# Kernel tuning notes

Hardware: AMD Instinct MI355X
Metric: run time of the kernel (lower is better)

## Reference

```python
import jax, jax.numpy as jnp
import numpy as np

B = 16      # number of point clouds in the batch
N = 2048    # points per cloud
P = B * N   # total points (flat PyG-style batching)
K = 16      # neighbors per point (col 0 = self loop)
OUT = 512   # out_channels


def _linear(key, fi, fo):
    # torch nn.Linear default init: U(-1/sqrt(fi), 1/sqrt(fi))
    s = 1.0 / np.sqrt(fi)
    kw, kb = jax.random.split(key)
    W = jax.random.uniform(kw, (fi, fo), jnp.float32, -s, s)
    b = jax.random.uniform(kb, (fo,), jnp.float32, -s, s)
    return W, b


def setup_inputs() -> dict:
    key = jax.random.key(0)
    ks = jax.random.split(key, 6)
    pos = jax.random.normal(ks[0], (P, 3), jnp.float32)
    # flat batch vector: points are grouped contiguously per cloud
    batch = (jnp.arange(P, dtype=jnp.int32) // N).astype(jnp.int32)
    # within-cloud random neighbor indices (stand-in for knn/radius graph)
    base = (jnp.arange(P) // N) * N  # offset of each point's cloud
    nbr = base[:, None] + jax.random.randint(ks[1], (P, K), 0, N)
    nbr = nbr.at[:, 0].set(jnp.arange(P))  # self loop (PyG add_self_loops)
    W1, b1 = _linear(ks[2], 3, 64)          # sa1 MLP layer 1
    W2, b2 = _linear(ks[3], 64, 128)        # sa1 MLP layer 2
    W3, b3 = _linear(ks[4], 128 + 3, 256)   # sa2 MLP layer 1
    W4, b4 = _linear(ks[5], 256, OUT)       # sa2 MLP layer 2
    return dict(pos=pos, nbr=nbr.astype(jnp.int64), batch=batch,
                W1=W1, b1=b1, W2=W2, b2=b2, W3=W3, b3=b3, W4=W4, b4=b4)


def reference(pos, nbr, batch, W1, b1, W2, b2, W3, b3, W4, b4):
    # ----- sa1: x is None -> message = MLP(pos_j - pos_i), max-aggregated -----
    diff = pos[nbr] - pos[:, None, :]                      # [P, K, 3]
    h1 = jnp.maximum(diff @ W1 + b1, 0.0) @ W2 + b2        # [P, K, 128]
    x1 = jnp.max(h1, axis=1)                               # [P, 128]
    # ----- sa2: message = MLP([x1_j, pos_j - pos_i]), max-aggregated -----
    feats = jnp.concatenate([x1[nbr], diff], axis=-1)      # [P, K, 131]
    h2 = jnp.maximum(feats @ W3 + b3, 0.0) @ W4 + b4       # [P, K, 512]
    x2 = jnp.max(h2, axis=1)                               # [P, 512]
    # ----- global_max_pool over batch -----
    return jax.ops.segment_max(x2, batch, num_segments=B)  # [B, 512]
```

## Files before the change

### kernel.cpp

```cpp
#include <hip/hip_runtime.h>
#include <hip/hip_bf16.h>

#define PTOT   32768
#define KNB    16
#define NCLOUD 16
#define OUTC   512
#define A1S    168
#define A2S    264

typedef __attribute__((ext_vector_type(8)))  short v8bf;
typedef __attribute__((ext_vector_type(16))) float v16f;

__device__ __forceinline__ unsigned short f2b(float v) {
    __hip_bfloat16 h = __float2bfloat16(v);
    return *reinterpret_cast<unsigned short*>(&h);
}
__device__ __forceinline__ unsigned pk2(float a, float b) {
    return (unsigned)f2b(a) | ((unsigned)f2b(b) << 16);
}
__device__ __forceinline__ unsigned fenc(float f) {
    unsigned u = __float_as_uint(f);
    return (u & 0x80000000u) ? ~u : (u | 0x80000000u);
}
__device__ __forceinline__ float fdec(unsigned u) {
    unsigned b = (u & 0x80000000u) ? (u & 0x7FFFFFFFu) : ~u;
    return __uint_as_float(b);
}
__device__ __forceinline__ v16f zero16() {
    v16f z;
    #pragma unroll
    for (int i = 0; i < 16; ++i) z[i] = 0.0f;
    return z;
}

__global__ void prep_kernel(const float* __restrict__ W1, const float* __restrict__ W2,
                            const float* __restrict__ W3, const float* __restrict__ W4,
                            unsigned short* __restrict__ W1s, unsigned short* __restrict__ W2s,
                            unsigned short* __restrict__ W3s, unsigned short* __restrict__ W4s)
{
    int i = blockIdx.x * 256 + threadIdx.x;
    if (i < 40960) {
        int j = i & 7, n = (i >> 3) & 255, c2 = i >> 11;
        int k = c2 * 8 + j;
        W3s[i] = f2b(k < 131 ? W3[k * 256 + n] : 0.0f);
    }
    int i2 = i - 40960;
    if (i2 >= 0 && i2 < 131072) {
        int j = i2 & 7, n = (i2 >> 3) & 511, c2 = i2 >> 12;
        int k = c2 * 8 + j;
        W4s[i2] = f2b(W4[k * 512 + n]);
    }
    int i3 = i - 172032;
    if (i3 >= 0 && i3 < 1024) {
        int k = i3 & 15, n = i3 >> 4;
        W1s[i3] = f2b(k < 3 ? W1[k * 64 + n] : 0.0f);
    }
    int i4 = i - 173056;
    if (i4 >= 0 && i4 < 8192) {
        int k = i4 & 63, n = i4 >> 6;
        W2s[i4] = f2b(W2[k * 128 + n]);
    }
}

__global__ __launch_bounds__(256) void sa1_kernel(
    const float* __restrict__ pos, const int* __restrict__ nbr,
    const unsigned short* __restrict__ W1s, const float* __restrict__ b1,
    const unsigned short* __restrict__ W2s, const float* __restrict__ b2,
    unsigned short* __restrict__ x1b)
{
    __shared__ unsigned short A1d[64 * 16];
    __shared__ unsigned short A2[64 * 72];
    const int tid  = threadIdx.x;
    const int lane = tid & 63;
    const int wave = tid >> 6;
    const int l31  = lane & 31;
    const int h    = lane >> 5;
    const int p0   = blockIdx.x * 4;

    if (tid < 64) {
        int r = tid;
        int j = nbr[p0 * KNB + r];
        int p = p0 + (r >> 4);
        v8bf z;
        #pragma unroll
        for (int i = 0; i < 8; ++i) z[i] = 0;
        v8bf dv = z;
        dv[0] = (short)f2b(pos[j * 3 + 0] - pos[p * 3 + 0]);
        dv[1] = (short)f2b(pos[j * 3 + 1] - pos[p * 3 + 1]);
        dv[2] = (short)f2b(pos[j * 3 + 2] - pos[p * 3 + 2]);
        *(v8bf*)(A1d + r * 16)     = dv;
        *(v8bf*)(A1d + r * 16 + 8) = z;
    }
    const int c1 = (wave >> 1) * 32 + l31;
    v8bf b1f = *(const v8bf*)(W1s + c1 * 16 + h * 8);
    const float b1v = b1[c1];
    __syncthreads();

    {
        v8bf a = *(const v8bf*)(A1d + ((wave & 1) * 32 + l31) * 16 + h * 8);
        v16f acc = __builtin_amdgcn_mfma_f32_32x32x16_bf16(a, b1f, zero16(), 0, 0, 0);
        #pragma unroll
        for (int r = 0; r < 16; ++r) {
            int row = (wave & 1) * 32 + (r & 3) + 8 * (r >> 2) + 4 * h;
            A2[row * 72 + c1] = f2b(fmaxf(acc[r] + b1v, 0.0f));
        }
    }
    v8bf B2[4];
    #pragma unroll
    for (int kc = 0; kc < 4; ++kc)
        B2[kc] = *(const v8bf*)(W2s + (wave * 32 + l31) * 64 + kc * 16 + h * 8);
    const float b2v = b2[wave * 32 + l31];
    __syncthreads();

    #pragma unroll
    for (int rt = 0; rt < 2; ++rt) {
        v16f acc = zero16();
        #pragma unroll
        for (int kc = 0; kc < 4; ++kc) {
            v8bf a = *(const v8bf*)(A2 + (rt * 32 + l31) * 72 + kc * 16 + h * 8);
            acc = __builtin_amdgcn_mfma_f32_32x32x16_bf16(a, B2[kc], acc, 0, 0, 0);
        }
        float ma = acc[0], mb = acc[8];
        #pragma unroll
        for (int r = 1; r < 8; ++r) { ma = fmaxf(ma, acc[r]); mb = fmaxf(mb, acc[8 + r]); }
        ma = fmaxf(ma, __shfl_xor(ma, 32));
        mb = fmaxf(mb, __shfl_xor(mb, 32));
        int p = p0 + rt * 2 + h;
        float m = h ? mb : ma;
        x1b[p * 128 + wave * 32 + l31] = f2b(m + b2v);
    }
}

__global__ __launch_bounds__(256) void sa2_kernel(
    const float* __restrict__ pos, const int* __restrict__ nbr,
    const int* __restrict__ batch,
    const unsigned short* __restrict__ W3s, const float* __restrict__ b3,
    const unsigned short* __restrict__ W4s, const float* __restrict__ b4,
    const unsigned short* __restrict__ x1b, unsigned* __restrict__ encbuf)
{
    __shared__ unsigned short S[128 * A2S];
    const int tid  = threadIdx.x;
    const int lane = tid & 63;
    const int wave = tid >> 6;
    const int l31  = lane & 31;
    const int h    = lane >> 5;
    const int p0   = blockIdx.x * 8;

    const float b3v0 = b3[(wave * 2 + 0) * 32 + l31];
    const float b3v1 = b3[(wave * 2 + 1) * 32 + l31];

    {
        int r = tid >> 1, q = tid & 1;
        int j = nbr[p0 * KNB + r];
        const uint4* src = (const uint4*)(x1b + j * 128 + q * 64);
        uint4* dst = (uint4*)(S + r * A1S + q * 64);
        #pragma unroll
        for (int i = 0; i < 8; ++i) dst[i] = src[i];
    }
    if (tid < 128) {
        int r = tid;
        int j = nbr[p0 * KNB + r];
        int p = p0 + (r >> 4);
        v8bf z;
        #pragma unroll
        for (int i = 0; i < 8; ++i) z[i] = 0;
        v8bf dv = z;
        dv[0] = (short)f2b(pos[j * 3 + 0] - pos[p * 3 + 0]);
        dv[1] = (short)f2b(pos[j * 3 + 1] - pos[p * 3 + 1]);
        dv[2] = (short)f2b(pos[j * 3 + 2] - pos[p * 3 + 2]);
        *(v8bf*)(S + r * A1S + 128) = dv;
        *(v8bf*)(S + r * A1S + 136) = z;
    }
    __syncthreads();

    const int n1a = (wave * 2 + 0) * 32 + l31;
    const int n1b = (wave * 2 + 1) * 32 + l31;
    unsigned stA[2][16], stB[2][16];
    #pragma unroll
    for (int rtp = 0; rtp < 2; ++rtp) {
        v16f g00 = zero16(), g01 = zero16(), g10 = zero16(), g11 = zero16();
        #pragma unroll
        for (int kc = 0; kc < 9; ++kc) {
            v8bf a0 = *(const v8bf*)(S + (rtp * 64 + l31)      * A1S + kc * 16 + h * 8);
            v8bf a1 = *(const v8bf*)(S + (rtp * 64 + 32 + l31) * A1S + kc * 16 + h * 8);
            int c2 = kc * 2 + h;
            v8bf B0 = *(const v8bf*)(W3s + ((c2 * 256 + n1a) << 3));
            v8bf B1 = *(const v8bf*)(W3s + ((c2 * 256 + n1b) << 3));
            g00 = __builtin_amdgcn_mfma_f32_32x32x16_bf16(a0, B0, g00, 0, 0, 0);
            g10 = __builtin_amdgcn_mfma_f32_32x32x16_bf16(a1, B0, g10, 0, 0, 0);
            g01 = __builtin_amdgcn_mfma_f32_32x32x16_bf16(a0, B1, g01, 0, 0, 0);
            g11 = __builtin_amdgcn_mfma_f32_32x32x16_bf16(a1, B1, g11, 0, 0, 0);
        }
        #pragma unroll
        for (int i = 0; i < 8; ++i) {
            stA[rtp][i]     = pk2(fmaxf(g00[2*i] + b3v0, 0.0f), fmaxf(g00[2*i+1] + b3v0, 0.0f));
            stA[rtp][8 + i] = pk2(fmaxf(g10[2*i] + b3v0, 0.0f), fmaxf(g10[2*i+1] + b3v0, 0.0f));
            stB[rtp][i]     = pk2(fmaxf(g01[2*i] + b3v1, 0.0f), fmaxf(g01[2*i+1] + b3v1, 0.0f));
            stB[rtp][8 + i] = pk2(fmaxf(g11[2*i] + b3v1, 0.0f), fmaxf(g11[2*i+1] + b3v1, 0.0f));
        }
    }
    __syncthreads();

    {
        const int c0 = (wave * 2 + 0) * 32 + l31;
        const int c1 = (wave * 2 + 1) * 32 + l31;
        #pragma unroll
        for (int rtp = 0; rtp < 2; ++rtp) {
            const int rb = rtp * 64;
            #pragma unroll
            for (int i = 0; i < 8; ++i) {
                int row = rb + ((2*i) & 3) + 8 * ((2*i) >> 2) + 4 * h;
                S[row * A2S + c0]        = (unsigned short)(stA[rtp][i] & 0xFFFF);
                S[(row + 1) * A2S + c0]  = (unsigned short)(stA[rtp][i] >> 16);
                S[(row + 32) * A2S + c0] = (unsigned short)(stA[rtp][8 + i] & 0xFFFF);
                S[(row + 33) * A2S + c0] = (unsigned short)(stA[rtp][8 + i] >> 16);
                S[row * A2S + c1]        = (unsigned short)(stB[rtp][i] & 0xFFFF);
                S[(row + 1) * A2S + c1]  = (unsigned short)(stB[rtp][i] >> 16);
                S[(row + 32) * A2S + c1] = (unsigned short)(stB[rtp][8 + i] & 0xFFFF);
                S[(row + 33) * A2S + c1] = (unsigned short)(stB[rtp][8 + i] >> 16);
            }
        }
    }
    __syncthreads();

    const int cloud = batch[p0];
    #pragma unroll
    for (int cp = 0; cp < 2; ++cp) {
        const int ct0 = wave * 4 + cp * 2;
        const int n0 = ct0 * 32 + l31;
        const int n1 = (ct0 + 1) * 32 + l31;
        v8bf B2a[16], B2b[16];
        #pragma unroll
        for (int kc = 0; kc < 16; ++kc) {
            int c2 = kc * 2 + h;
            B2a[kc] = *(const v8bf*)(W4s + ((c2 * 512 + n0) << 3));
            B2b[kc] = *(const v8bf*)(W4s + ((c2 * 512 + n1) << 3));
        }
        float rm0 = -3.4e38f, rm1 = -3.4e38f;
        #pragma unroll
        for (int rtp = 0; rtp < 2; ++rtp) {
            v16f a00 = zero16(), a01 = zero16(), a10 = zero16(), a11 = zero16();
            #pragma unroll
            for (int kc = 0; kc < 16; ++kc) {
                v8bf a0 = *(const v8bf*)(S + (rtp * 64 + l31)      * A2S + kc * 16 + h * 8);
                v8bf a1 = *(const v8bf*)(S + (rtp * 64 + 32 + l31) * A2S + kc * 16 + h * 8);
                a00 = __builtin_amdgcn_mfma_f32_32x32x16_bf16(a0, B2a[kc], a00, 0, 0, 0);
                a10 = __builtin_amdgcn_mfma_f32_32x32x16_bf16(a1, B2a[kc], a10, 0, 0, 0);
                a01 = __builtin_amdgcn_mfma_f32_32x32x16_bf16(a0, B2b[kc], a01, 0, 0, 0);
                a11 = __builtin_amdgcn_mfma_f32_32x32x16_bf16(a1, B2b[kc], a11, 0, 0, 0);
            }
            #pragma unroll
            for (int r = 0; r < 16; ++r) {
                rm0 = fmaxf(rm0, fmaxf(a00[r], a10[r]));
                rm1 = fmaxf(rm1, fmaxf(a01[r], a11[r]));
            }
        }
        rm0 = fmaxf(rm0, __shfl_xor(rm0, 32));
        rm1 = fmaxf(rm1, __shfl_xor(rm1, 32));
        rm0 += b4[ct0 * 32 + l31];
        rm1 += b4[(ct0 + 1) * 32 + l31];
        if (lane < 32) {
            atomicMax(&encbuf[cloud * OUTC + ct0 * 32 + l31], fenc(rm0));
            atomicMax(&encbuf[cloud * OUTC + (ct0 + 1) * 32 + l31], fenc(rm1));
        }
    }
}

__global__ void finalize_kernel(const unsigned* __restrict__ encv,
                                float* __restrict__ out)
{
    int i = blockIdx.x * 256 + threadIdx.x;
    if (i < NCLOUD * OUTC) out[i] = fdec(encv[i]);
}

extern "C" void kernel_launch(void* const* d_in, const int* in_sizes, int n_in,
                              void* d_out, int out_size, void* d_ws, size_t ws_size,
                              hipStream_t stream)
{
    const float* pos   = (const float*)d_in[0];
    const int*   nbr   = (const int*)  d_in[1];
    const int*   batch = (const int*)  d_in[2];
    const float* W1    = (const float*)d_in[3];
    const float* b1    = (const float*)d_in[4];
    const float* W2    = (const float*)d_in[5];
    const float* b2    = (const float*)d_in[6];
    const float* W3    = (const float*)d_in[7];
    const float* b3    = (const float*)d_in[8];
    const float* W4    = (const float*)d_in[9];
    const float* b4    = (const float*)d_in[10];

    unsigned short* x1b = (unsigned short*)d_ws;
    unsigned short* W3s = (unsigned short*)((char*)d_ws + 8388608);
    unsigned short* W4s = (unsigned short*)((char*)d_ws + 8470528);
    unsigned*    encbuf = (unsigned*)((char*)d_ws + 8732672);
    unsigned short* W1s = (unsigned short*)((char*)d_ws + 8765440);
    unsigned short* W2s = (unsigned short*)((char*)d_ws + 8767488);

    hipMemsetAsync(encbuf, 0, NCLOUD * OUTC * sizeof(unsigned), stream);
    prep_kernel<<<708, 256, 0, stream>>>(W1, W2, W3, W4, W1s, W2s, W3s, W4s);
    sa1_kernel<<<PTOT / 4, 256, 0, stream>>>(pos, nbr, W1s, b1, W2s, b2, x1b);
    sa2_kernel<<<PTOT / 8, 256, 0, stream>>>(pos, nbr, batch, W3s, b3, W4s, b4, x1b, encbuf);
    finalize_kernel<<<(NCLOUD * OUTC + 255) / 256, 256, 0, stream>>>(encbuf, (float*)d_out);
}
```

Before: 252.7 us.

## Make sa2 persistent over point tiles with register-resident W4 and prefetch

The sa2 kernel now uses 512 threads and processes four 8-point tiles per block. Each wave holds its W4 column slice in registers for all tiles and keeps running max accumulators, so W4 loads and atomicMax traffic happen once per block instead of once per tile. The next tile's gathered neighbor features are prefetched into registers while the current layer-2 MFMAs run, with separate LDS buffers for the layer-1 input and the hidden activations. The encbuf zeroing moves from a memset into prep_kernel to drop one launch. The trade-offs are higher register pressure (32 v8bf B fragments held live) and a quarter as many blocks.

```diff
diff --git a/kernel.cpp b/kernel.cpp
--- a/kernel.cpp
+++ b/kernel.cpp
@@ -7,6 +7,7 @@
 #define OUTC   512
 #define A1S    168
 #define A2S    264
+#define TTIL   4
 
 typedef __attribute__((ext_vector_type(8)))  short v8bf;
 typedef __attribute__((ext_vector_type(16))) float v16f;
@@ -14,9 +15,6 @@
 __device__ __forceinline__ unsigned short f2b(float v) {
     __hip_bfloat16 h = __float2bfloat16(v);
     return *reinterpret_cast<unsigned short*>(&h);
-}
-__device__ __forceinline__ unsigned pk2(float a, float b) {
-    return (unsigned)f2b(a) | ((unsigned)f2b(b) << 16);
 }
 __device__ __forceinline__ unsigned fenc(float f) {
     unsigned u = __float_as_uint(f);
@@ -36,9 +34,11 @@
 __global__ void prep_kernel(const float* __restrict__ W1, const float* __restrict__ W2,
                             const float* __restrict__ W3, const float* __restrict__ W4,
                             unsigned short* __restrict__ W1s, unsigned short* __restrict__ W2s,
-                            unsigned short* __restrict__ W3s, unsigned short* __restrict__ W4s)
+                            unsigned short* __restrict__ W3s, unsigned short* __restrict__ W4s,
+                            unsigned* __restrict__ encbuf)
 {
     int i = blockIdx.x * 256 + threadIdx.x;
+    if (i < NCLOUD * OUTC) encbuf[i] = 0u;
     if (i < 40960) {
         int j = i & 7, n = (i >> 3) & 255, c2 = i >> 11;
         int k = c2 * 8 + j;
@@ -131,138 +131,140 @@
     }
 }
 
-__global__ __launch_bounds__(256) void sa2_kernel(
+__global__ __launch_bounds__(512) void sa2_kernel(
     const float* __restrict__ pos, const int* __restrict__ nbr,
     const int* __restrict__ batch,
     const unsigned short* __restrict__ W3s, const float* __restrict__ b3,
     const unsigned short* __restrict__ W4s, const float* __restrict__ b4,
     const unsigned short* __restrict__ x1b, unsigned* __restrict__ encbuf)
 {
-    __shared__ unsigned short S[128 * A2S];
+    __shared__ unsigned short A1[128 * A1S];
+    __shared__ unsigned short A2[128 * A2S];
     const int tid  = threadIdx.x;
     const int lane = tid & 63;
     const int wave = tid >> 6;
     const int l31  = lane & 31;
     const int h    = lane >> 5;
-    const int p0   = blockIdx.x * 8;
-
-    const float b3v0 = b3[(wave * 2 + 0) * 32 + l31];
-    const float b3v1 = b3[(wave * 2 + 1) * 32 + l31];
+    const int pbase = blockIdx.x * (8 * TTIL);
+
+    const int n0 = (wave * 2 + 0) * 32 + l31;
+    const int n1 = (wave * 2 + 1) * 32 + l31;
+    v8bf B2a[16], B2b[16];
+    #pragma unroll
+    for (int kc = 0; kc < 16; ++kc) {
+        int c2 = kc * 2 + h;
+        B2a[kc] = *(const v8bf*)(W4s + ((c2 * 512 + n0) << 3));
+        B2b[kc] = *(const v8bf*)(W4s + ((c2 * 512 + n1) << 3));
+    }
+    const int cw = wave * 32 + l31;
+    const float b3v = b3[cw];
+
+    float rm0 = -3.4e38f, rm1 = -3.4e38f;
+    const int rs = tid >> 2, q4 = tid & 3;
 
     {
-        int r = tid >> 1, q = tid & 1;
-        int j = nbr[p0 * KNB + r];
-        const uint4* src = (const uint4*)(x1b + j * 128 + q * 64);
-        uint4* dst = (uint4*)(S + r * A1S + q * 64);
-        #pragma unroll
-        for (int i = 0; i < 8; ++i) dst[i] = src[i];
-    }
-    if (tid < 128) {
-        int r = tid;
-        int j = nbr[p0 * KNB + r];
-        int p = p0 + (r >> 4);
-        v8bf z;
-        #pragma unroll
-        for (int i = 0; i < 8; ++i) z[i] = 0;
-        v8bf dv = z;
-        dv[0] = (short)f2b(pos[j * 3 + 0] - pos[p * 3 + 0]);
-        dv[1] = (short)f2b(pos[j * 3 + 1] - pos[p * 3 + 1]);
-        dv[2] = (short)f2b(pos[j * 3 + 2] - pos[p * 3 + 2]);
-        *(v8bf*)(S + r * A1S + 128) = dv;
-        *(v8bf*)(S + r * A1S + 136) = z;
+        int j = nbr[pbase * KNB + rs];
+        const uint4* src = (const uint4*)(x1b + j * 128 + q4 * 32);
+        uint4* dst = (uint4*)(A1 + rs * A1S + q4 * 32);
+        dst[0] = src[0]; dst[1] = src[1]; dst[2] = src[2]; dst[3] = src[3];
+        if (tid < 128) {
+            int jj = nbr[pbase * KNB + tid];
+            int pp = pbase + (tid >> 4);
+            v8bf z;
+            #pragma unroll
+            for (int i = 0; i < 8; ++i) z[i] = 0;
+            v8bf dv = z;
+            dv[0] = (short)f2b(pos[jj * 3 + 0] - pos[pp * 3 + 0]);
+            dv[1] = (short)f2b(pos[jj * 3 + 1] - pos[pp * 3 + 1]);
+            dv[2] = (short)f2b(pos[jj * 3 + 2] - pos[pp * 3 + 2]);
+            *(v8bf*)(A1 + tid * A1S + 128) = dv;
+            *(v8bf*)(A1 + tid * A1S + 136) = z;
+        }
     }
     __syncthreads();
 
-    const int n1a = (wave * 2 + 0) * 32 + l31;
-    const int n1b = (wave * 2 + 1) * 32 + l31;
-    unsigned stA[2][16], stB[2][16];
-    #pragma unroll
-    for (int rtp = 0; rtp < 2; ++rtp) {
-        v16f g00 = zero16(), g01 = zero16(), g10 = zero16(), g11 = zero16();
+    for (int t = 0; t < TTIL; ++t) {
+        v8bf B1[9];
         #pragma unroll
         for (int kc = 0; kc < 9; ++kc) {
-            v8bf a0 = *(const v8bf*)(S + (rtp * 64 + l31)      * A1S + kc * 16 + h * 8);
-            v8bf a1 = *(const v8bf*)(S + (rtp * 64 + 32 + l31) * A1S + kc * 16 + h * 8);
             int c2 = kc * 2 + h;
-            v8bf B0 = *(const v8bf*)(W3s + ((c2 * 256 + n1a) << 3));
-            v8bf B1 = *(const v8bf*)(W3s + ((c2 * 256 + n1b) << 3));
-            g00 = __builtin_amdgcn_mfma_f32_32x32x16_bf16(a0, B0, g00, 0, 0, 0);
-            g10 = __builtin_amdgcn_mfma_f32_32x32x16_bf16(a1, B0, g10, 0, 0, 0);
-            g01 = __builtin_amdgcn_mfma_f32_32x32x16_bf16(a0, B1, g01, 0, 0, 0);
-            g11 = __builtin_amdgcn_mfma_f32_32x32x16_bf16(a1, B1, g11, 0, 0, 0);
-        }
-        #pragma unroll
-        for (int i = 0; i < 8; ++i) {
-            stA[rtp][i]     = pk2(fmaxf(g00[2*i] + b3v0, 0.0f), fmaxf(g00[2*i+1] + b3v0, 0.0f));
-            stA[rtp][8 + i] = pk2(fmaxf(g10[2*i] + b3v0, 0.0f), fmaxf(g10[2*i+1] + b3v0, 0.0f));
-            stB[rtp][i]     = pk2(fmaxf(g01[2*i] + b3v1, 0.0f), fmaxf(g01[2*i+1] + b3v1, 0.0f));
-            stB[rtp][8 + i] = pk2(fmaxf(g11[2*i] + b3v1, 0.0f), fmaxf(g11[2*i+1] + b3v1, 0.0f));
-        }
-    }
-    __syncthreads();
-
-    {
-        const int c0 = (wave * 2 + 0) * 32 + l31;
-        const int c1 = (wave * 2 + 1) * 32 + l31;
-        #pragma unroll
-        for (int rtp = 0; rtp < 2; ++rtp) {
-            const int rb = rtp * 64;
-            #pragma unroll
-            for (int i = 0; i < 8; ++i) {
-                int row = rb + ((2*i) & 3) + 8 * ((2*i) >> 2) + 4 * h;
-                S[row * A2S + c0]        = (unsigned short)(stA[rtp][i] & 0xFFFF);
-                S[(row + 1) * A2S + c0]  = (unsigned short)(stA[rtp][i] >> 16);
-                S[(row + 32) * A2S + c0] = (unsigned short)(stA[rtp][8 + i] & 0xFFFF);
-                S[(row + 33) * A2S + c0] = (unsigned short)(stA[rtp][8 + i] >> 16);
-                S[row * A2S + c1]        = (unsigned short)(stB[rtp][i] & 0xFFFF);
-                S[(row + 1) * A2S + c1]  = (unsigned short)(stB[rtp][i] >> 16);
-                S[(row + 32) * A2S + c1] = (unsigned short)(stB[rtp][8 + i] & 0xFFFF);
-                S[(row + 33) * A2S + c1] = (unsigned short)(stB[rtp][8 + i] >> 16);
-            }
-        }
-    }
-    __syncthreads();
-
-    const int cloud = batch[p0];
-    #pragma unroll
-    for (int cp = 0; cp < 2; ++cp) {
-        const int ct0 = wave * 4 + cp * 2;
-        const int n0 = ct0 * 32 + l31;
-        const int n1 = (ct0 + 1) * 32 + l31;
-        v8bf B2a[16], B2b[16];
-        #pragma unroll
-        for (int kc = 0; kc < 16; ++kc) {
-            int c2 = kc * 2 + h;
-            B2a[kc] = *(const v8bf*)(W4s + ((c2 * 512 + n0) << 3));
-            B2b[kc] = *(const v8bf*)(W4s + ((c2 * 512 + n1) << 3));
-        }
-        float rm0 = -3.4e38f, rm1 = -3.4e38f;
-        #pragma unroll
-        for (int rtp = 0; rtp < 2; ++rtp) {
-            v16f a00 = zero16(), a01 = zero16(), a10 = zero16(), a11 = zero16();
+            B1[kc] = *(const v8bf*)(W3s + ((c2 * 256 + cw) << 3));
+        }
+        #pragma unroll
+        for (int rt = 0; rt < 4; ++rt) {
+            v16f g = zero16();
+            #pragma unroll
+            for (int kc = 0; kc < 9; ++kc) {
+                v8bf a = *(const v8bf*)(A1 + (rt * 32 + l31) * A1S + kc * 16 + h * 8);
+                g = __builtin_amdgcn_mfma_f32_32x32x16_bf16(a, B1[kc], g, 0, 0, 0);
+            }
+            #pragma unroll
+            for (int i = 0; i < 16; ++i) {
+                int row = rt * 32 + (i & 3) + 8 * (i >> 2) + 4 * h;
+                A2[row * A2S + cw] = f2b(fmaxf(g[i] + b3v, 0.0f));
+            }
+        }
+        __syncthreads();
+
+        uint4 pv0, pv1, pv2, pv3;
+        float dx = 0.f, dy = 0.f, dz = 0.f;
+        const int have = (t + 1 < TTIL);
+        if (have) {
+            int p0n = pbase + (t + 1) * 8;
+            int j = nbr[p0n * KNB + rs];
+            const uint4* src = (const uint4*)(x1b + j * 128 + q4 * 32);
+            pv0 = src[0]; pv1 = src[1]; pv2 = src[2]; pv3 = src[3];
+            if (tid < 128) {
+                int jj = nbr[p0n * KNB + tid];
+                int pp = p0n + (tid >> 4);
+                dx = pos[jj * 3 + 0] - pos[pp * 3 + 0];
+                dy = pos[jj * 3 + 1] - pos[pp * 3 + 1];
+                dz = pos[jj * 3 + 2] - pos[pp * 3 + 2];
+            }
+        }
+
+        #pragma unroll
+        for (int rt = 0; rt < 4; ++rt) {
+            v16f a0 = zero16(), a1 = zero16();
             #pragma unroll
             for (int kc = 0; kc < 16; ++kc) {
-                v8bf a0 = *(const v8bf*)(S + (rtp * 64 + l31)      * A2S + kc * 16 + h * 8);
-                v8bf a1 = *(const v8bf*)(S + (rtp * 64 + 32 + l31) * A2S + kc * 16 + h * 8);
-                a00 = __builtin_amdgcn_mfma_f32_32x32x16_bf16(a0, B2a[kc], a00, 0, 0, 0);
-                a10 = __builtin_amdgcn_mfma_f32_32x32x16_bf16(a1, B2a[kc], a10, 0, 0, 0);
-                a01 = __builtin_amdgcn_mfma_f32_32x32x16_bf16(a0, B2b[kc], a01, 0, 0, 0);
-                a11 = __builtin_amdgcn_mfma_f32_32x32x16_bf16(a1, B2b[kc], a11, 0, 0, 0);
+                v8bf a = *(const v8bf*)(A2 + (rt * 32 + l31) * A2S + kc * 16 + h * 8);
+                a0 = __builtin_amdgcn_mfma_f32_32x32x16_bf16(a, B2a[kc], a0, 0, 0, 0);
+                a1 = __builtin_amdgcn_mfma_f32_32x32x16_bf16(a, B2b[kc], a1, 0, 0, 0);
             }
             #pragma unroll
             for (int r = 0; r < 16; ++r) {
-                rm0 = fmaxf(rm0, fmaxf(a00[r], a10[r]));
-                rm1 = fmaxf(rm1, fmaxf(a01[r], a11[r]));
-            }
-        }
-        rm0 = fmaxf(rm0, __shfl_xor(rm0, 32));
-        rm1 = fmaxf(rm1, __shfl_xor(rm1, 32));
-        rm0 += b4[ct0 * 32 + l31];
-        rm1 += b4[(ct0 + 1) * 32 + l31];
-        if (lane < 32) {
-            atomicMax(&encbuf[cloud * OUTC + ct0 * 32 + l31], fenc(rm0));
-            atomicMax(&encbuf[cloud * OUTC + (ct0 + 1) * 32 + l31], fenc(rm1));
-        }
+                rm0 = fmaxf(rm0, a0[r]);
+                rm1 = fmaxf(rm1, a1[r]);
+            }
+        }
+
+        if (have) {
+            uint4* dst = (uint4*)(A1 + rs * A1S + q4 * 32);
+            dst[0] = pv0; dst[1] = pv1; dst[2] = pv2; dst[3] = pv3;
+            if (tid < 128) {
+                v8bf z;
+                #pragma unroll
+                for (int i = 0; i < 8; ++i) z[i] = 0;
+                v8bf dv = z;
+                dv[0] = (short)f2b(dx);
+                dv[1] = (short)f2b(dy);
+                dv[2] = (short)f2b(dz);
+                *(v8bf*)(A1 + tid * A1S + 128) = dv;
+                *(v8bf*)(A1 + tid * A1S + 136) = z;
+            }
+        }
+        __syncthreads();
+    }
+
+    rm0 = fmaxf(rm0, __shfl_xor(rm0, 32));
+    rm1 = fmaxf(rm1, __shfl_xor(rm1, 32));
+    rm0 += b4[n0];
+    rm1 += b4[n1];
+    const int cloud = batch[pbase];
+    if (lane < 32) {
+        atomicMax(&encbuf[cloud * OUTC + n0], fenc(rm0));
+        atomicMax(&encbuf[cloud * OUTC + n1], fenc(rm1));
     }
 }
 
@@ -296,9 +298,8 @@
     unsigned short* W1s = (unsigned short*)((char*)d_ws + 8765440);
     unsigned short* W2s = (unsigned short*)((char*)d_ws + 8767488);
 
-    hipMemsetAsync(encbuf, 0, NCLOUD * OUTC * sizeof(unsigned), stream);
-    prep_kernel<<<708, 256, 0, stream>>>(W1, W2, W3, W4, W1s, W2s, W3s, W4s);
+    prep_kernel<<<708, 256, 0, stream>>>(W1, W2, W3, W4, W1s, W2s, W3s, W4s, encbuf);
     sa1_kernel<<<PTOT / 4, 256, 0, stream>>>(pos, nbr, W1s, b1, W2s, b2, x1b);
-    sa2_kernel<<<PTOT / 8, 256, 0, stream>>>(pos, nbr, batch, W3s, b3, W4s, b4, x1b, encbuf);
+    sa2_kernel<<<PTOT / (8 * TTIL), 512, 0, stream>>>(pos, nbr, batch, W3s, b3, W4s, b4, x1b, encbuf);
     finalize_kernel<<<(NCLOUD * OUTC + 255) / 256, 256, 0, stream>>>(encbuf, (float*)d_out);
 }
```

After: 523.5 us. 107% more time.

## Restructure sa2 MFMA tiling to 4 row tiles x 4 column tiles per wave

Applied to the files above, without the earlier changes.

Rewrites the sa2 GEMM loops so each wave keeps all 128 rows (4 row tiles) in flight and loads each B fragment once per k-chunk. The second GEMM now holds a 4x4 accumulator grid instead of two passes over two column pairs, so W4 fragments are read from global memory only once per block and all atomics are issued together. The launch bound is set to one block per CU to allow the larger register footprint (256 accumulator VGPRs), at the cost of occupancy. The encbuf memset is also folded into prep_kernel, removing one launch.

```diff
diff --git a/kernel.cpp b/kernel.cpp
--- a/kernel.cpp
+++ b/kernel.cpp
@@ -36,9 +36,11 @@
 __global__ void prep_kernel(const float* __restrict__ W1, const float* __restrict__ W2,
                             const float* __restrict__ W3, const float* __restrict__ W4,
                             unsigned short* __restrict__ W1s, unsigned short* __restrict__ W2s,
-                            unsigned short* __restrict__ W3s, unsigned short* __restrict__ W4s)
+                            unsigned short* __restrict__ W3s, unsigned short* __restrict__ W4s,
+                            unsigned* __restrict__ encbuf)
 {
     int i = blockIdx.x * 256 + threadIdx.x;
+    if (i < NCLOUD * OUTC) encbuf[i] = 0u;
     if (i < 40960) {
         int j = i & 7, n = (i >> 3) & 255, c2 = i >> 11;
         int k = c2 * 8 + j;
@@ -131,7 +133,7 @@
     }
 }
 
-__global__ __launch_bounds__(256) void sa2_kernel(
+__global__ __launch_bounds__(256, 1) void sa2_kernel(
     const float* __restrict__ pos, const int* __restrict__ nbr,
     const int* __restrict__ batch,
     const unsigned short* __restrict__ W3s, const float* __restrict__ b3,
@@ -146,9 +148,6 @@
     const int h    = lane >> 5;
     const int p0   = blockIdx.x * 8;
 
-    const float b3v0 = b3[(wave * 2 + 0) * 32 + l31];
-    const float b3v1 = b3[(wave * 2 + 1) * 32 + l31];
-
     {
         int r = tid >> 1, q = tid & 1;
         int j = nbr[p0 * KNB + r];
@@ -175,94 +174,90 @@
 
     const int n1a = (wave * 2 + 0) * 32 + l31;
     const int n1b = (wave * 2 + 1) * 32 + l31;
-    unsigned stA[2][16], stB[2][16];
-    #pragma unroll
-    for (int rtp = 0; rtp < 2; ++rtp) {
-        v16f g00 = zero16(), g01 = zero16(), g10 = zero16(), g11 = zero16();
-        #pragma unroll
-        for (int kc = 0; kc < 9; ++kc) {
-            v8bf a0 = *(const v8bf*)(S + (rtp * 64 + l31)      * A1S + kc * 16 + h * 8);
-            v8bf a1 = *(const v8bf*)(S + (rtp * 64 + 32 + l31) * A1S + kc * 16 + h * 8);
-            int c2 = kc * 2 + h;
-            v8bf B0 = *(const v8bf*)(W3s + ((c2 * 256 + n1a) << 3));
-            v8bf B1 = *(const v8bf*)(W3s + ((c2 * 256 + n1b) << 3));
-            g00 = __builtin_amdgcn_mfma_f32_32x32x16_bf16(a0, B0, g00, 0, 0, 0);
-            g10 = __builtin_amdgcn_mfma_f32_32x32x16_bf16(a1, B0, g10, 0, 0, 0);
-            g01 = __builtin_amdgcn_mfma_f32_32x32x16_bf16(a0, B1, g01, 0, 0, 0);
-            g11 = __builtin_amdgcn_mfma_f32_32x32x16_bf16(a1, B1, g11, 0, 0, 0);
-        }
+    v16f g[4][2];
+    #pragma unroll
+    for (int rt = 0; rt < 4; ++rt) { g[rt][0] = zero16(); g[rt][1] = zero16(); }
+    #pragma unroll
+    for (int kc = 0; kc < 9; ++kc) {
+        int c2 = kc * 2 + h;
+        v8bf B0 = *(const v8bf*)(W3s + ((c2 * 256 + n1a) << 3));
+        v8bf B1 = *(const v8bf*)(W3s + ((c2 * 256 + n1b) << 3));
+        #pragma unroll
+        for (int rt = 0; rt < 4; ++rt) {
+            v8bf a = *(const v8bf*)(S + (rt * 32 + l31) * A1S + kc * 16 + h * 8);
+            g[rt][0] = __builtin_amdgcn_mfma_f32_32x32x16_bf16(a, B0, g[rt][0], 0, 0, 0);
+            g[rt][1] = __builtin_amdgcn_mfma_f32_32x32x16_bf16(a, B1, g[rt][1], 0, 0, 0);
+        }
+    }
+    const float b3v0 = b3[n1a];
+    const float b3v1 = b3[n1b];
+    unsigned st[4][2][8];
+    #pragma unroll
+    for (int rt = 0; rt < 4; ++rt) {
         #pragma unroll
         for (int i = 0; i < 8; ++i) {
-            stA[rtp][i]     = pk2(fmaxf(g00[2*i] + b3v0, 0.0f), fmaxf(g00[2*i+1] + b3v0, 0.0f));
-            stA[rtp][8 + i] = pk2(fmaxf(g10[2*i] + b3v0, 0.0f), fmaxf(g10[2*i+1] + b3v0, 0.0f));
-            stB[rtp][i]     = pk2(fmaxf(g01[2*i] + b3v1, 0.0f), fmaxf(g01[2*i+1] + b3v1, 0.0f));
-            stB[rtp][8 + i] = pk2(fmaxf(g11[2*i] + b3v1, 0.0f), fmaxf(g11[2*i+1] + b3v1, 0.0f));
-        }
-    }
-    __syncthreads();
-
-    {
-        const int c0 = (wave * 2 + 0) * 32 + l31;
-        const int c1 = (wave * 2 + 1) * 32 + l31;
-        #pragma unroll
-        for (int rtp = 0; rtp < 2; ++rtp) {
-            const int rb = rtp * 64;
+            st[rt][0][i] = pk2(fmaxf(g[rt][0][2*i] + b3v0, 0.0f), fmaxf(g[rt][0][2*i+1] + b3v0, 0.0f));
+            st[rt][1][i] = pk2(fmaxf(g[rt][1][2*i] + b3v1, 0.0f), fmaxf(g[rt][1][2*i+1] + b3v1, 0.0f));
+        }
+    }
+    __syncthreads();
+
+    #pragma unroll
+    for (int rt = 0; rt < 4; ++rt) {
+        #pragma unroll
+        for (int i = 0; i < 8; ++i) {
+            int row = rt * 32 + ((2*i) & 3) + 8 * ((2*i) >> 2) + 4 * h;
+            S[row * A2S + n1a]       = (unsigned short)(st[rt][0][i] & 0xFFFF);
+            S[(row + 1) * A2S + n1a] = (unsigned short)(st[rt][0][i] >> 16);
+            S[row * A2S + n1b]       = (unsigned short)(st[rt][1][i] & 0xFFFF);
+            S[(row + 1) * A2S + n1b] = (unsigned short)(st[rt][1][i] >> 16);
+        }
+    }
+    __syncthreads();
+
+    const int nc0 = (wave * 4 + 0) * 32 + l31;
+    const int nc1 = (wave * 4 + 1) * 32 + l31;
+    const int nc2 = (wave * 4 + 2) * 32 + l31;
+    const int nc3 = (wave * 4 + 3) * 32 + l31;
+    v16f acc[4][4];
+    #pragma unroll
+    for (int rt = 0; rt < 4; ++rt)
+        #pragma unroll
+        for (int c = 0; c < 4; ++c) acc[rt][c] = zero16();
+    #pragma unroll
+    for (int kc = 0; kc < 16; ++kc) {
+        int c2 = kc * 2 + h;
+        v8bf B0 = *(const v8bf*)(W4s + ((c2 * 512 + nc0) << 3));
+        v8bf B1 = *(const v8bf*)(W4s + ((c2 * 512 + nc1) << 3));
+        v8bf B2 = *(const v8bf*)(W4s + ((c2 * 512 + nc2) << 3));
+        v8bf B3 = *(const v8bf*)(W4s + ((c2 * 512 + nc3) << 3));
+        #pragma unroll
+        for (int rt = 0; rt < 4; ++rt) {
+            v8bf a = *(const v8bf*)(S + (rt * 32 + l31) * A2S + kc * 16 + h * 8);
+            acc[rt][0] = __builtin_amdgcn_mfma_f32_32x32x16_bf16(a, B0, acc[rt][0], 0, 0, 0);
+            acc[rt][1] = __builtin_amdgcn_mfma_f32_32x32x16_bf16(a, B1, acc[rt][1], 0, 0, 0);
+            acc[rt][2] = __builtin_amdgcn_mfma_f32_32x32x16_bf16(a, B2, acc[rt][2], 0, 0, 0);
+            acc[rt][3] = __builtin_amdgcn_mfma_f32_32x32x16_bf16(a, B3, acc[rt][3], 0, 0, 0);
+        }
+    }
+
+    float rm[4];
+    #pragma unroll
+    for (int c = 0; c < 4; ++c) {
+        float m = acc[0][c][0];
+        #pragma unroll
+        for (int rt = 0; rt < 4; ++rt)
             #pragma unroll
-            for (int i = 0; i < 8; ++i) {
-                int row = rb + ((2*i) & 3) + 8 * ((2*i) >> 2) + 4 * h;
-                S[row * A2S + c0]        = (unsigned short)(stA[rtp][i] & 0xFFFF);
-                S[(row + 1) * A2S + c0]  = (unsigned short)(stA[rtp][i] >> 16);
-                S[(row + 32) * A2S + c0] = (unsigned short)(stA[rtp][8 + i] & 0xFFFF);
-                S[(row + 33) * A2S + c0] = (unsigned short)(stA[rtp][8 + i] >> 16);
-                S[row * A2S + c1]        = (unsigned short)(stB[rtp][i] & 0xFFFF);
-                S[(row + 1) * A2S + c1]  = (unsigned short)(stB[rtp][i] >> 16);
-                S[(row + 32) * A2S + c1] = (unsigned short)(stB[rtp][8 + i] & 0xFFFF);
-                S[(row + 33) * A2S + c1] = (unsigned short)(stB[rtp][8 + i] >> 16);
-            }
-        }
-    }
-    __syncthreads();
-
+            for (int r = 0; r < 16; ++r) m = fmaxf(m, acc[rt][c][r]);
+        rm[c] = fmaxf(m, __shfl_xor(m, 32));
+    }
     const int cloud = batch[p0];
-    #pragma unroll
-    for (int cp = 0; cp < 2; ++cp) {
-        const int ct0 = wave * 4 + cp * 2;
-        const int n0 = ct0 * 32 + l31;
-        const int n1 = (ct0 + 1) * 32 + l31;
-        v8bf B2a[16], B2b[16];
-        #pragma unroll
-        for (int kc = 0; kc < 16; ++kc) {
-            int c2 = kc * 2 + h;
-            B2a[kc] = *(const v8bf*)(W4s + ((c2 * 512 + n0) << 3));
-            B2b[kc] = *(const v8bf*)(W4s + ((c2 * 512 + n1) << 3));
-        }
-        float rm0 = -3.4e38f, rm1 = -3.4e38f;
-        #pragma unroll
-        for (int rtp = 0; rtp < 2; ++rtp) {
-            v16f a00 = zero16(), a01 = zero16(), a10 = zero16(), a11 = zero16();
-            #pragma unroll
-            for (int kc = 0; kc < 16; ++kc) {
-                v8bf a0 = *(const v8bf*)(S + (rtp * 64 + l31)      * A2S + kc * 16 + h * 8);
-                v8bf a1 = *(const v8bf*)(S + (rtp * 64 + 32 + l31) * A2S + kc * 16 + h * 8);
-                a00 = __builtin_amdgcn_mfma_f32_32x32x16_bf16(a0, B2a[kc], a00, 0, 0, 0);
-                a10 = __builtin_amdgcn_mfma_f32_32x32x16_bf16(a1, B2a[kc], a10, 0, 0, 0);
-                a01 = __builtin_amdgcn_mfma_f32_32x32x16_bf16(a0, B2b[kc], a01, 0, 0, 0);
-                a11 = __builtin_amdgcn_mfma_f32_32x32x16_bf16(a1, B2b[kc], a11, 0, 0, 0);
-            }
-            #pragma unroll
-            for (int r = 0; r < 16; ++r) {
-                rm0 = fmaxf(rm0, fmaxf(a00[r], a10[r]));
-                rm1 = fmaxf(rm1, fmaxf(a01[r], a11[r]));
-            }
-        }
-        rm0 = fmaxf(rm0, __shfl_xor(rm0, 32));
-        rm1 = fmaxf(rm1, __shfl_xor(rm1, 32));
-        rm0 += b4[ct0 * 32 + l31];
-        rm1 += b4[(ct0 + 1) * 32 + l31];
-        if (lane < 32) {
-            atomicMax(&encbuf[cloud * OUTC + ct0 * 32 + l31], fenc(rm0));
-            atomicMax(&encbuf[cloud * OUTC + (ct0 + 1) * 32 + l31], fenc(rm1));
-        }
+    rm[0] += b4[nc0]; rm[1] += b4[nc1]; rm[2] += b4[nc2]; rm[3] += b4[nc3];
+    if (lane < 32) {
+        atomicMax(&encbuf[cloud * OUTC + nc0], fenc(rm[0]));
+        atomicMax(&encbuf[cloud * OUTC + nc1], fenc(rm[1]));
+        atomicMax(&encbuf[cloud * OUTC + nc2], fenc(rm[2]));
+        atomicMax(&encbuf[cloud * OUTC + nc3], fenc(rm[3]));
     }
 }
 
@@ -296,8 +291,7 @@
     unsigned short* W1s = (unsigned short*)((char*)d_ws + 8765440);
     unsigned short* W2s = (unsigned short*)((char*)d_ws + 8767488);
 
-    hipMemsetAsync(encbuf, 0, NCLOUD * OUTC * sizeof(unsigned), stream);
-    prep_kernel<<<708, 256, 0, stream>>>(W1, W2, W3, W4, W1s, W2s, W3s, W4s);
+    prep_kernel<<<708, 256, 0, stream>>>(W1, W2, W3, W4, W1s, W2s, W3s, W4s, encbuf);
     sa1_kernel<<<PTOT / 4, 256, 0, stream>>>(pos, nbr, W1s, b1, W2s, b2, x1b);
     sa2_kernel<<<PTOT / 8, 256, 0, stream>>>(pos, nbr, batch, W3s, b3, W4s, b4, x1b, encbuf);
     finalize_kernel<<<(NCLOUD * OUTC + 255) / 256, 256, 0, stream>>>(encbuf, (float*)d_out);
```

Result: slower. 286.6 us (+13.4%).
